# Performance work log

Measured on AMD Instinct MI355X. Metric: run time of the kernel, lower is better.

## Reference

```python
import jax, jax.numpy as jnp
import numpy as np

B, N, F_IN, D, TOPK, HID = 64, 512, 256, 128, 20, 512


def setup_inputs() -> dict:
    key = jax.random.key(0)
    ks = jax.random.split(key, 10)
    s = lambda fan: 1.0 / np.sqrt(fan)
    return {
        "data": jax.random.normal(ks[0], (B, F_IN, N), jnp.float32),
        "emb_weight": jax.random.normal(ks[1], (N, D), jnp.float32) * s(D),      # nn.Embedding, kaiming-ish
        "lin_w": jax.random.normal(ks[2], (D, F_IN), jnp.float32) * s(F_IN),     # GraphLayer.lin (no bias)
        "att_i": jax.random.normal(ks[3], (D,), jnp.float32) * 0.1,
        "att_j": jax.random.normal(ks[4], (D,), jnp.float32) * 0.1,
        "att_em_i": jax.random.normal(ks[5], (D,), jnp.float32) * 0.1,
        "att_em_j": jax.random.normal(ks[6], (D,), jnp.float32) * 0.1,
        "gnn_bias": jnp.zeros((D,), jnp.float32),
        "bn_gamma": jnp.ones((D,), jnp.float32),
        "bn_beta": jnp.zeros((D,), jnp.float32),
        "w1": jax.random.normal(ks[7], (HID, N), jnp.float32) * s(N),            # Linear(node_num, hidden, bias=False)
        "w2": jax.random.normal(ks[8], (HID, HID), jnp.float32) * s(HID),        # Linear(hidden, hidden)
        "b2": jnp.zeros((HID,), jnp.float32),
    }


def reference(data, emb_weight, lin_w, att_i, att_j, att_em_i, att_em_j,
              gnn_bias, bn_gamma, bn_beta, w1, w2, b2):
    data = jax.lax.stop_gradient(data)                       # x = data.clone().detach()
    b, f_in, n = data.shape
    d = emb_weight.shape[1]
    x = jnp.transpose(data, (0, 2, 1)).reshape(b * n, f_in)  # [B*N, F]

    # --- dynamic graph from detached embedding: cosine topk ---
    W = jax.lax.stop_gradient(emb_weight)
    nrm = jnp.linalg.norm(W, axis=-1)
    cos = (W @ W.T) / (nrm[:, None] * nrm[None, :])
    topk_idx = jax.lax.top_k(cos, TOPK)[1]                   # [N, topk] (learned_graph)
    src = topk_idx.reshape(-1)                               # gated_j (sources)
    dst = jnp.repeat(jnp.arange(n), TOPK)                    # gated_i (destinations)
    offs = (jnp.arange(b) * n)[:, None]
    bsrc = (src[None, :] + offs).reshape(-1)                 # [B*N*topk]
    bdst = (dst[None, :] + offs).reshape(-1)

    # --- GDN GraphLayer (heads=1, concat=False, aggr=add) ---
    xl = x @ lin_w.T                                         # [B*N, D]
    emb_all = jnp.tile(emb_weight, (b, 1))                   # [B*N, D]
    xi, xj = xl[bdst], xl[bsrc]
    ei, ej = emb_all[bdst], emb_all[bsrc]
    alpha = xi @ att_i + ei @ att_em_i + xj @ att_j + ej @ att_em_j   # [E]
    alpha = jax.nn.leaky_relu(alpha, 0.2)
    amax = jax.ops.segment_max(alpha, bdst, num_segments=b * n)
    ex = jnp.exp(alpha - amax[bdst])
    denom = jax.ops.segment_sum(ex, bdst, num_segments=b * n)
    a = ex / denom[bdst]                                     # segment softmax over dest
    agg = jax.ops.segment_sum(xj * a[:, None], bdst, num_segments=b * n) + gnn_bias

    # --- BatchNorm1d (eval: mean 0, var 1) + ReLU ---
    h = agg * (bn_gamma / jnp.sqrt(1.0 + 1e-5)) + bn_beta
    gcn = jax.nn.relu(h).reshape(b, n, d)

    # --- embedding gate + linear block over node dim ---
    out = gcn * emb_weight[None]                             # [B, N, D]
    out = jnp.transpose(out, (0, 2, 1))                      # [B, D, N]
    out = out @ w1.T                                         # [B, D, HID]
    out = out @ w2.T + b2
    out = jax.nn.sigmoid(out)
    return out, emb_weight, topk_idx
```

## Files before the change

kernel.cpp:

```cpp
#include <hip/hip_runtime.h>
#include <hip/hip_bf16.h>

constexpr int B = 64, N = 512, F_IN = 256, D = 128, TOPK = 20, HID = 512;

typedef __attribute__((ext_vector_type(8))) short short8_t;
typedef __attribute__((ext_vector_type(4))) float f32x4;

__device__ inline short f2bs(float f) {
    union { __hip_bfloat16 h; short s; } u; u.h = __float2bfloat16(f); return u.s;
}
__device__ inline float bs2f(short s) {
    return __uint_as_float(((unsigned)(unsigned short)s) << 16);
}

template<int ITERS>
__device__ inline void stage_bf16(short* ldst, const short* __restrict__ src,
                                  int stride, int k0, int t) {
    #pragma unroll
    for (int i = 0; i < ITERS; ++i) {
        int lin = t + i * 256, row = lin >> 2, seg = lin & 3;
        *(short8_t*)&ldst[row * 40 + seg * 8] =
            *(const short8_t*)&src[(size_t)row * stride + k0 + seg * 8];
    }
}
template<int ITERS>
__device__ inline void stage_f32(short* ldst, const float* __restrict__ src,
                                 int stride, int k0, int t) {
    #pragma unroll
    for (int i = 0; i < ITERS; ++i) {
        int lin = t + i * 256, row = lin >> 2, seg = lin & 3;
        const float* p = &src[(size_t)row * stride + k0 + seg * 8];
        float4 x = *(const float4*)p, y = *(const float4*)(p + 4);
        short8_t v = { f2bs(x.x), f2bs(x.y), f2bs(x.z), f2bs(x.w),
                       f2bs(y.x), f2bs(y.y), f2bs(y.z), f2bs(y.w) };
        *(short8_t*)&ldst[row * 40 + seg * 8] = v;
    }
}

template<int MS, int NS>
__device__ inline void mfma_tiles(const short* lds_a, const short* lds_b,
                                  f32x4 (&acc)[MS][NS], int wm, int wn, int lr, int quad) {
    short8_t af[MS], bf[NS];
    #pragma unroll
    for (int ms = 0; ms < MS; ++ms)
        af[ms] = *(const short8_t*)&lds_a[(wm + ms * 16 + lr) * 40 + quad * 8];
    #pragma unroll
    for (int ns = 0; ns < NS; ++ns)
        bf[ns] = *(const short8_t*)&lds_b[(wn + ns * 16 + lr) * 40 + quad * 8];
    #pragma unroll
    for (int ms = 0; ms < MS; ++ms)
        #pragma unroll
        for (int ns = 0; ns < NS; ++ns)
            acc[ms][ns] = __builtin_amdgcn_mfma_f32_16x16x32_bf16(af[ms], bf[ns], acc[ms][ns], 0, 0, 0);
}

__global__ void k_norm(const float* __restrict__ W, const float* __restrict__ aei,
                       const float* __restrict__ aej, float* __restrict__ inv_norm,
                       float* __restrict__ ei, float* __restrict__ ej,
                       float* __restrict__ out_emb) {
    int n = blockIdx.x, t = threadIdx.x;
    float w = W[n * D + t];
    out_emb[n * D + t] = w;
    float s0 = w * w, s1 = w * aei[t], s2 = w * aej[t];
    #pragma unroll
    for (int o = 32; o > 0; o >>= 1) {
        s0 += __shfl_down(s0, o); s1 += __shfl_down(s1, o); s2 += __shfl_down(s2, o);
    }
    __shared__ float r[6];
    if ((t & 63) == 0) { int q = t >> 6; r[q * 3] = s0; r[q * 3 + 1] = s1; r[q * 3 + 2] = s2; }
    __syncthreads();
    if (t == 0) {
        inv_norm[n] = 1.0f / sqrtf(r[0] + r[3]);
        ei[n] = r[1] + r[4];
        ej[n] = r[2] + r[5];
    }
}

__global__ __launch_bounds__(256) void k_cos(const float* __restrict__ W,
                                             const float* __restrict__ inv_norm,
                                             float* __restrict__ cosm) {
    __shared__ float la[32][33];
    __shared__ float lb[32][33];
    int j0 = blockIdx.x * 32, i0 = blockIdx.y * 32, t = threadIdx.x;
    int ix = (t & 15) * 2, jx = (t >> 4) * 2;
    float acc[2][2] = {};
    for (int k0 = 0; k0 < D; k0 += 32) {
        #pragma unroll
        for (int i = 0; i < 4; ++i) {
            int lin = t + i * 256, rl = lin & 31, kk = lin >> 5;
            la[kk][rl] = W[(size_t)(i0 + rl) * D + k0 + kk];
            lb[kk][rl] = W[(size_t)(j0 + rl) * D + k0 + kk];
        }
        __syncthreads();
        #pragma unroll
        for (int kk = 0; kk < 32; ++kk) {
            float a0 = la[kk][ix], a1 = la[kk][ix + 1];
            float b0 = lb[kk][jx], b1 = lb[kk][jx + 1];
            acc[0][0] += a0 * b0; acc[0][1] += a0 * b1;
            acc[1][0] += a1 * b0; acc[1][1] += a1 * b1;
        }
        __syncthreads();
    }
    #pragma unroll
    for (int ii = 0; ii < 2; ++ii) {
        float inv_i = inv_norm[i0 + ix + ii];
        float2 v;
        v.x = acc[ii][0] * inv_i * inv_norm[j0 + jx + 0];
        v.y = acc[ii][1] * inv_i * inv_norm[j0 + jx + 1];
        *(float2*)&cosm[(size_t)(i0 + ix + ii) * N + j0 + jx] = v;
    }
}

__global__ __launch_bounds__(256) void k_sel(const float* __restrict__ cosm,
                                             int* __restrict__ topk,
                                             float* __restrict__ out_idx) {
    int t = threadIdx.x, wid = t >> 6, lane = t & 63;
    int i = blockIdx.x * 4 + wid;
    float4 p0 = *(const float4*)&cosm[(size_t)i * N + lane * 8];
    float4 p1 = *(const float4*)&cosm[(size_t)i * N + lane * 8 + 4];
    float v[8] = {p0.x, p0.y, p0.z, p0.w, p1.x, p1.y, p1.z, p1.w};
    for (int k = 0; k < TOPK; ++k) {
        float bv = v[0]; int bc = 0;
        #pragma unroll
        for (int c = 1; c < 8; ++c) if (v[c] > bv) { bv = v[c]; bc = c; }
        int bj = lane * 8 + bc;
        #pragma unroll
        for (int o = 1; o < 64; o <<= 1) {
            float ov = __shfl_xor(bv, o);
            int  oj = __shfl_xor(bj, o);
            if (ov > bv || (ov == bv && oj < bj)) { bv = ov; bj = oj; }
        }
        if (lane == 0) {
            topk[i * TOPK + k] = bj;
            out_idx[i * TOPK + k] = (float)bj;
        }
        int oc = bj & 7; bool owner = (bj >> 3) == lane;
        #pragma unroll
        for (int c = 0; c < 8; ++c) if (owner && c == oc) v[c] = -INFINITY;
    }
}

__global__ __launch_bounds__(256) void k_transD(const float* __restrict__ data,
                                                short* __restrict__ dataT) {
    __shared__ float lt[32][33];
    int f0 = blockIdx.x * 32, n0 = blockIdx.y * 32, b = blockIdx.z, t = threadIdx.x;
    {
        int f = t >> 3, ng = (t & 7) * 4;
        float4 v = *(const float4*)&data[((size_t)b * F_IN + f0 + f) * N + n0 + ng];
        lt[f][ng] = v.x; lt[f][ng + 1] = v.y; lt[f][ng + 2] = v.z; lt[f][ng + 3] = v.w;
    }
    __syncthreads();
    {
        int n = t >> 3, fg = (t & 7) * 4;
        short4 w;
        w.x = f2bs(lt[fg + 0][n]); w.y = f2bs(lt[fg + 1][n]);
        w.z = f2bs(lt[fg + 2][n]); w.w = f2bs(lt[fg + 3][n]);
        *(short4*)&dataT[((size_t)b * N + n0 + n) * F_IN + f0 + fg] = w;
    }
}

__global__ __launch_bounds__(256) void k_xl(const short* __restrict__ dataT,
                                            const float* __restrict__ lin_w,
                                            short* __restrict__ xlb) {
    __shared__ __align__(16) short lds_a[64 * 40];
    __shared__ __align__(16) short lds_b[128 * 40];
    int n0 = blockIdx.x * 64, b = blockIdx.y, t = threadIdx.x;
    int wid = t >> 6, lane = t & 63;
    int wm = (wid & 1) * 32, wn = (wid >> 1) * 64;
    int lr = lane & 15, quad = lane >> 4;
    f32x4 acc[2][4] = {};
    const short* Asrc = dataT + ((size_t)b * N + n0) * F_IN;
    for (int k0 = 0; k0 < F_IN; k0 += 32) {
        stage_bf16<1>(lds_a, Asrc, F_IN, k0, t);
        stage_f32<2>(lds_b, lin_w, F_IN, k0, t);
        __syncthreads();
        mfma_tiles<2, 4>(lds_a, lds_b, acc, wm, wn, lr, quad);
        __syncthreads();
    }
    #pragma unroll
    for (int ms = 0; ms < 2; ++ms)
        #pragma unroll
        for (int ns = 0; ns < 4; ++ns) {
            int mb = wm + ms * 16 + quad * 4, col = wn + ns * 16 + lr;
            #pragma unroll
            for (int r = 0; r < 4; ++r)
                xlb[((size_t)b * N + n0 + mb + r) * D + col] = f2bs(acc[ms][ns][r]);
        }
}

__global__ __launch_bounds__(256) void k_scores(const short* __restrict__ xlb,
                                                const float* __restrict__ att_i,
                                                const float* __restrict__ att_j,
                                                const float* __restrict__ ei,
                                                const float* __restrict__ ej,
                                                float* __restrict__ s_i,
                                                float* __restrict__ s_j) {
    int t = threadIdx.x, wid = t >> 6, lane = t & 63;
    int v = blockIdx.x * 4 + wid;
    int n = v & (N - 1);
    unsigned x2 = *(const unsigned*)&xlb[(size_t)v * D + lane * 2];
    float x0 = __uint_as_float((x2 & 0xFFFFu) << 16);
    float x1 = __uint_as_float(x2 & 0xFFFF0000u);
    float2 ai = *(const float2*)&att_i[lane * 2];
    float2 aj = *(const float2*)&att_j[lane * 2];
    float si = x0 * ai.x + x1 * ai.y;
    float sj = x0 * aj.x + x1 * aj.y;
    #pragma unroll
    for (int o = 32; o > 0; o >>= 1) { si += __shfl_down(si, o); sj += __shfl_down(sj, o); }
    if (lane == 0) { s_i[v] = si + ei[n]; s_j[v] = sj + ej[n]; }
}

__global__ __launch_bounds__(256) void k_attn2(const short* __restrict__ xlb,
                                               const float* __restrict__ emb,
                                               const int* __restrict__ topk,
                                               const float* __restrict__ s_i,
                                               const float* __restrict__ s_j,
                                               const float* __restrict__ gnn_bias,
                                               const float* __restrict__ bn_gamma,
                                               const float* __restrict__ bn_beta,
                                               short* __restrict__ Gt) {
    __shared__ float alph[16][20];
    __shared__ int   js[16][20];
    __shared__ float lt[16][129];
    int n0 = blockIdx.x * 16, b = blockIdx.y, t = threadIdx.x;
    for (int e = t; e < 16 * TOPK; e += 256) {
        int nl = e / TOPK, k = e - nl * TOPK;
        int j = topk[(n0 + nl) * TOPK + k];
        js[nl][k] = j;
        float al = s_i[b * N + n0 + nl] + s_j[b * N + j];
        alph[nl][k] = al >= 0.f ? al : 0.2f * al;
    }
    __syncthreads();
    if (t < 16) {
        float m = -INFINITY;
        for (int k = 0; k < TOPK; ++k) m = fmaxf(m, alph[t][k]);
        float s = 0.f;
        for (int k = 0; k < TOPK; ++k) { float e_ = expf(alph[t][k] - m); alph[t][k] = e_; s += e_; }
        float inv = 1.0f / s;
        for (int k = 0; k < TOPK; ++k) alph[t][k] *= inv;
    }
    __syncthreads();
    {
        int nl = t >> 4, dl = (t & 15) * 8;
        float a[8] = {};
        for (int k = 0; k < TOPK; ++k) {
            float w = alph[nl][k];
            short8_t xv = *(const short8_t*)&xlb[((size_t)b * N + js[nl][k]) * D + dl];
            #pragma unroll
            for (int c = 0; c < 8; ++c) a[c] += w * bs2f(xv[c]);
        }
        const float bnk = 0.9999950000374997f;
        #pragma unroll
        for (int c = 0; c < 8; ++c) {
            int d = dl + c;
            float h = (a[c] + gnn_bias[d]) * (bn_gamma[d] * bnk) + bn_beta[d];
            h = fmaxf(h, 0.f);
            lt[nl][d] = h * emb[(n0 + nl) * D + d];
        }
    }
    __syncthreads();
    {
        int d = t >> 1, half = t & 1;
        short8_t v;
        #pragma unroll
        for (int j = 0; j < 8; ++j) v[j] = f2bs(lt[half * 8 + j][d]);
        *(short8_t*)&Gt[((size_t)b * D + d) * N + n0 + half * 8] = v;
    }
}

__global__ __launch_bounds__(256) void k_gemm1(const short* __restrict__ Gt,
                                               const float* __restrict__ w1,
                                               short* __restrict__ out1) {
    __shared__ __align__(16) short lds_a[128 * 40];
    __shared__ __align__(16) short lds_b[64 * 40];
    int h0 = blockIdx.x * 64, b = blockIdx.y, t = threadIdx.x;
    int wid = t >> 6, lane = t & 63;
    int wm = (wid >> 1) * 64, wn = (wid & 1) * 32;
    int lr = lane & 15, quad = lane >> 4;
    f32x4 acc[4][2] = {};
    const short* Asrc = Gt + (size_t)b * D * N;
    const float* Bsrc = w1 + (size_t)h0 * N;
    for (int k0 = 0; k0 < N; k0 += 32) {
        stage_bf16<2>(lds_a, Asrc, N, k0, t);
        stage_f32<1>(lds_b, Bsrc, N, k0, t);
        __syncthreads();
        mfma_tiles<4, 2>(lds_a, lds_b, acc, wm, wn, lr, quad);
        __syncthreads();
    }
    #pragma unroll
    for (int ms = 0; ms < 4; ++ms)
        #pragma unroll
        for (int ns = 0; ns < 2; ++ns) {
            int mb = wm + ms * 16 + quad * 4, col = h0 + wn + ns * 16 + lr;
            #pragma unroll
            for (int r = 0; r < 4; ++r)
                out1[((size_t)b * D + mb + r) * HID + col] = f2bs(acc[ms][ns][r]);
        }
}

__global__ __launch_bounds__(256) void k_gemm2(const short* __restrict__ out1,
                                               const float* __restrict__ w2,
                                               const float* __restrict__ b2,
                                               float* __restrict__ out) {
    __shared__ __align__(16) short lds_a[128 * 40];
    __shared__ __align__(16) short lds_b[64 * 40];
    int h0 = blockIdx.x * 64, b = blockIdx.y, t = threadIdx.x;
    int wid = t >> 6, lane = t & 63;
    int wm = (wid >> 1) * 64, wn = (wid & 1) * 32;
    int lr = lane & 15, quad = lane >> 4;
    f32x4 acc[4][2] = {};
    const short* Asrc = out1 + (size_t)b * D * HID;
    const float* Bsrc = w2 + (size_t)h0 * HID;
    for (int k0 = 0; k0 < HID; k0 += 32) {
        stage_bf16<2>(lds_a, Asrc, HID, k0, t);
        stage_f32<1>(lds_b, Bsrc, HID, k0, t);
        __syncthreads();
        mfma_tiles<4, 2>(lds_a, lds_b, acc, wm, wn, lr, quad);
        __syncthreads();
    }
    #pragma unroll
    for (int ms = 0; ms < 4; ++ms)
        #pragma unroll
        for (int ns = 0; ns < 2; ++ns) {
            int mb = wm + ms * 16 + quad * 4, col = h0 + wn + ns * 16 + lr;
            float bias = b2[col];
            #pragma unroll
            for (int r = 0; r < 4; ++r)
                out[((size_t)b * D + mb + r) * HID + col] =
                    1.0f / (1.0f + expf(-(acc[ms][ns][r] + bias)));
        }
}

extern "C" void kernel_launch(void* const* d_in, const int* in_sizes, int n_in,
                              void* d_out, int out_size, void* d_ws, size_t ws_size,
                              hipStream_t stream) {
    const float* data     = (const float*)d_in[0];
    const float* emb      = (const float*)d_in[1];
    const float* lin_w    = (const float*)d_in[2];
    const float* att_i    = (const float*)d_in[3];
    const float* att_j    = (const float*)d_in[4];
    const float* att_em_i = (const float*)d_in[5];
    const float* att_em_j = (const float*)d_in[6];
    const float* gnn_bias = (const float*)d_in[7];
    const float* bn_gamma = (const float*)d_in[8];
    const float* bn_beta  = (const float*)d_in[9];
    const float* w1       = (const float*)d_in[10];
    const float* w2       = (const float*)d_in[11];
    const float* b2       = (const float*)d_in[12];
    float* out            = (float*)d_out;

    float* ws       = (float*)d_ws;
    float* inv_norm = ws;
    float* ei       = ws + 512;
    float* ej       = ws + 1024;
    int*   topk     = (int*)(ws + 1536);
    float* s_i      = ws + 1536 + N * TOPK;
    float* s_j      = s_i + B * N;
    short* dataT    = (short*)(ws + 77312);
    float* cosm     = (float*)dataT;
    short* Gt       = dataT;
    short* out1     = dataT + (size_t)B * D * N;
    short* xlb      = dataT + (size_t)B * N * F_IN;

    float* out_emb = out + (size_t)B * D * HID;
    float* out_idx = out_emb + (size_t)N * D;

    hipLaunchKernelGGL(k_norm,   dim3(N),              dim3(D),   0, stream, emb, att_em_i, att_em_j, inv_norm, ei, ej, out_emb);
    hipLaunchKernelGGL(k_cos,    dim3(N / 32, N / 32), dim3(256), 0, stream, emb, inv_norm, cosm);
    hipLaunchKernelGGL(k_sel,    dim3(N / 4),          dim3(256), 0, stream, cosm, topk, out_idx);
    hipLaunchKernelGGL(k_transD, dim3(F_IN / 32, N / 32, B), dim3(256), 0, stream, data, dataT);
    hipLaunchKernelGGL(k_xl,     dim3(N / 64, B),      dim3(256), 0, stream, dataT, lin_w, xlb);
    hipLaunchKernelGGL(k_scores, dim3(B * N / 4),      dim3(256), 0, stream, xlb, att_i, att_j, ei, ej, s_i, s_j);
    hipLaunchKernelGGL(k_attn2,  dim3(N / 16, B),      dim3(256), 0, stream, xlb, emb, topk, s_i, s_j, gnn_bias, bn_gamma, bn_beta, Gt);
    hipLaunchKernelGGL(k_gemm1,  dim3(HID / 64, B),    dim3(256), 0, stream, Gt, w1, out1);
    hipLaunchKernelGGL(k_gemm2,  dim3(HID / 64, B),    dim3(256), 0, stream, out1, w2, b2, out);
}
```

Before: 201.0 us.

## Fuse transpose and attention-score computation into the xl GEMM kernel

```diff
diff --git a/kernel.cpp b/kernel.cpp
--- a/kernel.cpp
+++ b/kernel.cpp
@@ -140,39 +140,42 @@
     }
 }
 
-__global__ __launch_bounds__(256) void k_transD(const float* __restrict__ data,
-                                                short* __restrict__ dataT) {
-    __shared__ float lt[32][33];
-    int f0 = blockIdx.x * 32, n0 = blockIdx.y * 32, b = blockIdx.z, t = threadIdx.x;
-    {
-        int f = t >> 3, ng = (t & 7) * 4;
-        float4 v = *(const float4*)&data[((size_t)b * F_IN + f0 + f) * N + n0 + ng];
-        lt[f][ng] = v.x; lt[f][ng + 1] = v.y; lt[f][ng + 2] = v.z; lt[f][ng + 3] = v.w;
-    }
-    __syncthreads();
-    {
-        int n = t >> 3, fg = (t & 7) * 4;
-        short4 w;
-        w.x = f2bs(lt[fg + 0][n]); w.y = f2bs(lt[fg + 1][n]);
-        w.z = f2bs(lt[fg + 2][n]); w.w = f2bs(lt[fg + 3][n]);
-        *(short4*)&dataT[((size_t)b * N + n0 + n) * F_IN + f0 + fg] = w;
-    }
-}
-
-__global__ __launch_bounds__(256) void k_xl(const short* __restrict__ dataT,
+__global__ __launch_bounds__(256) void k_xl(const float* __restrict__ data,
                                             const float* __restrict__ lin_w,
-                                            short* __restrict__ xlb) {
+                                            const float* __restrict__ att_i,
+                                            const float* __restrict__ att_j,
+                                            const float* __restrict__ ei,
+                                            const float* __restrict__ ej,
+                                            short* __restrict__ xlb,
+                                            float* __restrict__ s_i,
+                                            float* __restrict__ s_j) {
+    __shared__ float lt[32][65];
     __shared__ __align__(16) short lds_a[64 * 40];
     __shared__ __align__(16) short lds_b[128 * 40];
+    __shared__ float sred[2][64][2];
     int n0 = blockIdx.x * 64, b = blockIdx.y, t = threadIdx.x;
     int wid = t >> 6, lane = t & 63;
     int wm = (wid & 1) * 32, wn = (wid >> 1) * 64;
     int lr = lane & 15, quad = lane >> 4;
     f32x4 acc[2][4] = {};
-    const short* Asrc = dataT + ((size_t)b * N + n0) * F_IN;
     for (int k0 = 0; k0 < F_IN; k0 += 32) {
-        stage_bf16<1>(lds_a, Asrc, F_IN, k0, t);
+        {
+            int f = t >> 3, ng = (t & 7) * 8;
+            const float* p = &data[((size_t)b * F_IN + k0 + f) * N + n0 + ng];
+            float4 v0 = *(const float4*)p, v1 = *(const float4*)(p + 4);
+            float* q = &lt[f][ng];
+            q[0] = v0.x; q[1] = v0.y; q[2] = v0.z; q[3] = v0.w;
+            q[4] = v1.x; q[5] = v1.y; q[6] = v1.z; q[7] = v1.w;
+        }
         stage_f32<2>(lds_b, lin_w, F_IN, k0, t);
+        __syncthreads();
+        {
+            int row = t >> 2, seg = t & 3;
+            short8_t a;
+            #pragma unroll
+            for (int j = 0; j < 8; ++j) a[j] = f2bs(lt[seg * 8 + j][row]);
+            *(short8_t*)&lds_a[row * 40 + seg * 8] = a;
+        }
         __syncthreads();
         mfma_tiles<2, 4>(lds_a, lds_b, acc, wm, wn, lr, quad);
         __syncthreads();
@@ -186,28 +189,45 @@
             for (int r = 0; r < 4; ++r)
                 xlb[((size_t)b * N + n0 + mb + r) * D + col] = f2bs(acc[ms][ns][r]);
         }
-}
-
-__global__ __launch_bounds__(256) void k_scores(const short* __restrict__ xlb,
-                                                const float* __restrict__ att_i,
-                                                const float* __restrict__ att_j,
-                                                const float* __restrict__ ei,
-                                                const float* __restrict__ ej,
-                                                float* __restrict__ s_i,
-                                                float* __restrict__ s_j) {
-    int t = threadIdx.x, wid = t >> 6, lane = t & 63;
-    int v = blockIdx.x * 4 + wid;
-    int n = v & (N - 1);
-    unsigned x2 = *(const unsigned*)&xlb[(size_t)v * D + lane * 2];
-    float x0 = __uint_as_float((x2 & 0xFFFFu) << 16);
-    float x1 = __uint_as_float(x2 & 0xFFFF0000u);
-    float2 ai = *(const float2*)&att_i[lane * 2];
-    float2 aj = *(const float2*)&att_j[lane * 2];
-    float si = x0 * ai.x + x1 * ai.y;
-    float sj = x0 * aj.x + x1 * aj.y;
-    #pragma unroll
-    for (int o = 32; o > 0; o >>= 1) { si += __shfl_down(si, o); sj += __shfl_down(sj, o); }
-    if (lane == 0) { s_i[v] = si + ei[n]; s_j[v] = sj + ej[n]; }
+    float si8[8], sj8[8];
+    #pragma unroll
+    for (int ms = 0; ms < 2; ++ms)
+        #pragma unroll
+        for (int r = 0; r < 4; ++r) {
+            float si = 0.f, sj = 0.f;
+            #pragma unroll
+            for (int ns = 0; ns < 4; ++ns) {
+                int col = wn + ns * 16 + lr;
+                float x = acc[ms][ns][r];
+                si += x * att_i[col];
+                sj += x * att_j[col];
+            }
+            si8[ms * 4 + r] = si; sj8[ms * 4 + r] = sj;
+        }
+    #pragma unroll
+    for (int o = 1; o < 16; o <<= 1) {
+        #pragma unroll
+        for (int i = 0; i < 8; ++i) {
+            si8[i] += __shfl_xor(si8[i], o);
+            sj8[i] += __shfl_xor(sj8[i], o);
+        }
+    }
+    if (lr == 0) {
+        #pragma unroll
+        for (int ms = 0; ms < 2; ++ms)
+            #pragma unroll
+            for (int r = 0; r < 4; ++r) {
+                int row = wm + ms * 16 + quad * 4 + r;
+                sred[wid >> 1][row][0] = si8[ms * 4 + r];
+                sred[wid >> 1][row][1] = sj8[ms * 4 + r];
+            }
+    }
+    __syncthreads();
+    if (t < 64) {
+        int n = n0 + t;
+        s_i[b * N + n] = sred[0][t][0] + sred[1][t][0] + ei[n];
+        s_j[b * N + n] = sred[0][t][1] + sred[1][t][1] + ej[n];
+    }
 }
 
 __global__ __launch_bounds__(256) void k_attn2(const short* __restrict__ xlb,
@@ -356,22 +376,20 @@
     int*   topk     = (int*)(ws + 1536);
     float* s_i      = ws + 1536 + N * TOPK;
     float* s_j      = s_i + B * N;
-    short* dataT    = (short*)(ws + 77312);
-    float* cosm     = (float*)dataT;
-    short* Gt       = dataT;
-    short* out1     = dataT + (size_t)B * D * N;
-    short* xlb      = dataT + (size_t)B * N * F_IN;
+    short* S        = (short*)(ws + 77312);
+    short* Gt       = S;
+    short* out1     = S + (size_t)B * D * N;
+    short* xlb      = S + 2 * (size_t)B * D * N;
+    float* cosm     = (float*)S;
 
     float* out_emb = out + (size_t)B * D * HID;
     float* out_idx = out_emb + (size_t)N * D;
 
-    hipLaunchKernelGGL(k_norm,   dim3(N),              dim3(D),   0, stream, emb, att_em_i, att_em_j, inv_norm, ei, ej, out_emb);
-    hipLaunchKernelGGL(k_cos,    dim3(N / 32, N / 32), dim3(256), 0, stream, emb, inv_norm, cosm);
-    hipLaunchKernelGGL(k_sel,    dim3(N / 4),          dim3(256), 0, stream, cosm, topk, out_idx);
-    hipLaunchKernelGGL(k_transD, dim3(F_IN / 32, N / 32, B), dim3(256), 0, stream, data, dataT);
-    hipLaunchKernelGGL(k_xl,     dim3(N / 64, B),      dim3(256), 0, stream, dataT, lin_w, xlb);
-    hipLaunchKernelGGL(k_scores, dim3(B * N / 4),      dim3(256), 0, stream, xlb, att_i, att_j, ei, ej, s_i, s_j);
-    hipLaunchKernelGGL(k_attn2,  dim3(N / 16, B),      dim3(256), 0, stream, xlb, emb, topk, s_i, s_j, gnn_bias, bn_gamma, bn_beta, Gt);
-    hipLaunchKernelGGL(k_gemm1,  dim3(HID / 64, B),    dim3(256), 0, stream, Gt, w1, out1);
-    hipLaunchKernelGGL(k_gemm2,  dim3(HID / 64, B),    dim3(256), 0, stream, out1, w2, b2, out);
-}
+    hipLaunchKernelGGL(k_norm,  dim3(N),              dim3(D),   0, stream, emb, att_em_i, att_em_j, inv_norm, ei, ej, out_emb);
+    hipLaunchKernelGGL(k_cos,   dim3(N / 32, N / 32), dim3(256), 0, stream, emb, inv_norm, cosm);
+    hipLaunchKernelGGL(k_sel,   dim3(N / 4),          dim3(256), 0, stream, cosm, topk, out_idx);
+    hipLaunchKernelGGL(k_xl,    dim3(N / 64, B),      dim3(256), 0, stream, data, lin_w, att_i, att_j, ei, ej, xlb, s_i, s_j);
+    hipLaunchKernelGGL(k_attn2, dim3(N / 16, B),      dim3(256), 0, stream, xlb, emb, topk, s_i, s_j, gnn_bias, bn_gamma, bn_beta, Gt);
+    hipLaunchKernelGGL(k_gemm1, dim3(HID / 64, B),    dim3(256), 0, stream, Gt, w1, out1);
+    hipLaunchKernelGGL(k_gemm2, dim3(HID / 64, B),    dim3(256), 0, stream, out1, w2, b2, out);
+}
```

After: 189.8 us. 5.6% less time.
